# Performance work log

Hardware: AMD Instinct MI355X
Metric: run time of the kernel (lower is better)

The kernel has to match this reference:

```python
import jax, jax.numpy as jnp
import numpy as np
from jax import lax

N, D_IN, D_H, D_A, N_CLS, K = 50000, 1024, 512, 256, 2, 8


def setup_inputs() -> dict:
    key = jax.random.key(0)
    ks = jax.random.split(key, 13)
    s = 0.02
    return {
        "h": jax.random.normal(ks[0], (1, N, D_IN), dtype=jnp.float32),
        "fc_W": jax.random.normal(ks[1], (D_H, D_IN), dtype=jnp.float32) * s,
        "fc_b": jnp.zeros((D_H,), jnp.float32),
        "att_a_W": jax.random.normal(ks[2], (D_A, D_H), dtype=jnp.float32) * s,
        "att_a_b": jnp.zeros((D_A,), jnp.float32),
        "att_b_W": jax.random.normal(ks[3], (D_A, D_H), dtype=jnp.float32) * s,
        "att_b_b": jnp.zeros((D_A,), jnp.float32),
        "att_c_W": jax.random.normal(ks[4], (1, D_A), dtype=jnp.float32) * s,
        "att_c_b": jnp.zeros((1,), jnp.float32),
        "cls_W": jax.random.normal(ks[5], (N_CLS, D_H), dtype=jnp.float32) * s,
        "cls_b": jnp.zeros((N_CLS,), jnp.float32),
        "inst_W": jax.random.normal(ks[6], (2, D_H), dtype=jnp.float32) * s,
        "inst_b": jnp.zeros((2,), jnp.float32),
        "label": 1,  # one_hot -> [0,1]: inst_eval runs only for classifier index 1
    }


def reference(h, fc_W, fc_b, att_a_W, att_a_b, att_b_W, att_b_b,
              att_c_W, att_c_b, cls_W, cls_b, inst_W, inst_b, label):
    x = jnp.squeeze(h, 0)                               # [N, 1024]
    hh = jax.nn.relu(x @ fc_W.T + fc_b)                 # [N, 512]
    # gated attention: tanh gate * sigmoid gate -> scalar score per instance
    a = jnp.tanh(hh @ att_a_W.T + att_a_b)              # [N, 256]
    b = jax.nn.sigmoid(hh @ att_b_W.T + att_b_b)        # [N, 256]
    A_raw = (a * b) @ att_c_W.T + att_c_b               # [N, 1]
    A = jax.nn.softmax(A_raw, axis=0)                   # softmax over instances

    # instance eval (label==1, subtyping=False -> only classifier index 1)
    scores = A_raw[:, 0]                                # [N]
    _, top_p_ids = lax.top_k(scores, K)
    _, top_n_ids = lax.top_k(-scores, K)
    ids = jnp.concatenate([top_p_ids, top_n_ids])       # [2K]
    inst = hh[ids]                                      # gather [2K, 512]
    logits = inst @ inst_W.T + inst_b                   # [2K, 2]
    targets = jnp.concatenate([jnp.ones((K,), jnp.int32),
                               jnp.zeros((K,), jnp.int32)])
    logp = jax.nn.log_softmax(logits, axis=-1)
    instance_loss = -jnp.mean(jnp.take_along_axis(logp, targets[:, None], axis=1))

    instance_scores = hh @ cls_W.T + cls_b              # [N, 2]
    preds = (instance_scores * A).sum(axis=0) / A.sum(axis=0)  # [2]
    preds = preds[None, :]                              # [1, 2]
    return preds, instance_scores, A_raw, instance_loss
```

## Files before the change

### kernel.cpp

```cpp
#include <hip/hip_runtime.h>
#include <hip/hip_bf16.h>
#include <math.h>

typedef __bf16 bf16_t;
typedef __bf16 bf16x4 __attribute__((ext_vector_type(4)));
typedef __bf16 bf16x8 __attribute__((ext_vector_type(8)));
typedef float  f32x4  __attribute__((ext_vector_type(4)));

#define NROWS 50000

typedef const __attribute__((address_space(1))) unsigned int* gp_t;
typedef __attribute__((address_space(3))) unsigned int* lp_t;
__device__ __forceinline__ void cp16(void* l, const void* g) {
    __builtin_amdgcn_global_load_lds((gp_t)g, (lp_t)l, 16, 0, 0);
}

__global__ void k_convert(const float* __restrict__ fcW,
                          const float* __restrict__ aW,
                          const float* __restrict__ bW,
                          const float* __restrict__ clsW,
                          bf16_t* __restrict__ permW1, bf16_t* __restrict__ permB2,
                          bf16_t* __restrict__ clsWb) {
    int t = blockIdx.x * 256 + threadIdx.x;
    if (t < 131072) {
        float4 v = *(const float4*)(fcW + (long)t * 4);
        int row = t >> 8;
        int k0 = (t & 255) * 4;
        int kt = k0 >> 5, q = (k0 >> 3) & 3, j = k0 & 7;
        bf16_t o[4] = {(bf16_t)v.x, (bf16_t)v.y, (bf16_t)v.z, (bf16_t)v.w};
        *(bf16x4*)(permW1 + kt * 16384 + q * 4096 + row * 8 + j) = *(bf16x4*)o;
    } else if (t < 196608) {
        int t2 = t - 131072;
        int isB = t2 >> 15;
        int f = t2 & 32767;
        float4 v = *(const float4*)(((isB ? bW : aW)) + (long)f * 4);
        int srow = f >> 7;
        int k0 = (f & 127) * 4;
        int kt = k0 >> 5, q = (k0 >> 3) & 3, j = k0 & 7;
        int r = ((srow >> 4) * 2 + isB) * 16 + (srow & 15);
        bf16_t o[4] = {(bf16_t)v.x, (bf16_t)v.y, (bf16_t)v.z, (bf16_t)v.w};
        *(bf16x4*)(permB2 + kt * 16384 + q * 4096 + r * 8 + j) = *(bf16x4*)o;
    } else if (t < 197632) {
        int i = t - 196608;
        clsWb[i] = (bf16_t)clsW[i];
    }
}

__global__ __launch_bounds__(256, 4) void k_gemm1(
        const float* __restrict__ x, const bf16_t* __restrict__ permW1,
        const float* __restrict__ fcb, bf16_t* __restrict__ hh) {
    __shared__ __align__(16) char smem[32768];
    const int tid = threadIdx.x;
    const int w = tid >> 6, l = tid & 63, q = l >> 4, li = l & 15;
    const int wr = w >> 1, wc = w & 1;
    const int b = blockIdx.x;
    const int rtile = (b & 7) | ((b >> 5) << 3);
    const int ctile = (b >> 3) & 3;
    const long row0 = (long)rtile * 128;
    const int col0 = ctile * 128;

    f32x4 acc[4][4];
    #pragma unroll
    for (int a = 0; a < 4; a++)
        #pragma unroll
        for (int c = 0; c < 4; c++) acc[a][c] = (f32x4)0.0f;

    int arow[4], akx[4]; bool avalid[4];
    #pragma unroll
    for (int j = 0; j < 4; j++) {
        int s = j * 256 + tid;
        arow[j] = s >> 3; akx[j] = s & 7;
        avalid[j] = (row0 + arow[j]) < NROWS;
    }
    const float* xbase = x + row0 * 1024;

    float4 xv[4];
    #pragma unroll
    for (int j = 0; j < 4; j++)
        xv[j] = avalid[j] ? *(const float4*)(xbase + arow[j] * 1024 + akx[j] * 4)
                          : make_float4(0.f, 0.f, 0.f, 0.f);
    #pragma unroll
    for (int j = 0; j < 4; j++) {
        bf16_t o[4] = {(bf16_t)xv[j].x, (bf16_t)xv[j].y, (bf16_t)xv[j].z, (bf16_t)xv[j].w};
        *(bf16x4*)(smem + (akx[j] >> 1) * 2048 + arow[j] * 16 + (akx[j] & 1) * 8) = *(bf16x4*)o;
    }
    #pragma unroll
    for (int s2 = 0; s2 < 2; s2++) {
        int s = tid + s2 * 256;
        cp16(smem + 16384 + s * 16, permW1 + (s >> 7) * 4096 + (col0 + (s & 127)) * 8);
    }
    #pragma unroll
    for (int j = 0; j < 4; j++)
        xv[j] = avalid[j] ? *(const float4*)(xbase + arow[j] * 1024 + 32 + akx[j] * 4)
                          : make_float4(0.f, 0.f, 0.f, 0.f);
    __syncthreads();

    for (int kt = 0; kt < 32; kt++) {
        const int cur = kt & 1, nxt = cur ^ 1;
        if (kt < 31) {
            const bf16_t* gsrc = permW1 + (long)(kt + 1) * 16384;
            #pragma unroll
            for (int s2 = 0; s2 < 2; s2++) {
                int s = tid + s2 * 256;
                cp16(smem + 16384 + nxt * 8192 + s * 16, gsrc + (s >> 7) * 4096 + (col0 + (s & 127)) * 8);
            }
            #pragma unroll
            for (int j = 0; j < 4; j++) {
                bf16_t o[4] = {(bf16_t)xv[j].x, (bf16_t)xv[j].y, (bf16_t)xv[j].z, (bf16_t)xv[j].w};
                *(bf16x4*)(smem + nxt * 8192 + (akx[j] >> 1) * 2048 + arow[j] * 16 + (akx[j] & 1) * 8) = *(bf16x4*)o;
            }
            int kn = (kt < 30 ? kt + 2 : 31) * 32;
            #pragma unroll
            for (int j = 0; j < 4; j++)
                xv[j] = avalid[j] ? *(const float4*)(xbase + arow[j] * 1024 + kn + akx[j] * 4)
                                  : make_float4(0.f, 0.f, 0.f, 0.f);
        }
        const bf16_t* Ab = (const bf16_t*)(smem + cur * 8192);
        const bf16_t* Bb = (const bf16_t*)(smem + 16384 + cur * 8192);
        bf16x8 afr[4], bfr[4];
        #pragma unroll
        for (int tn = 0; tn < 4; tn++)
            bfr[tn] = *(const bf16x8*)(Bb + q * 1024 + (wc * 64 + tn * 16 + li) * 8);
        #pragma unroll
        for (int tm = 0; tm < 4; tm++)
            afr[tm] = *(const bf16x8*)(Ab + q * 1024 + (wr * 64 + tm * 16 + li) * 8);
        #pragma unroll
        for (int tm = 0; tm < 4; tm++)
            #pragma unroll
            for (int tn = 0; tn < 4; tn++)
                acc[tm][tn] = __builtin_amdgcn_mfma_f32_16x16x32_bf16(afr[tm], bfr[tn], acc[tm][tn], 0, 0, 0);
        __syncthreads();
    }

    bf16_t* t16 = (bf16_t*)smem;
    float bias[4];
    #pragma unroll
    for (int tn = 0; tn < 4; tn++) bias[tn] = fcb[col0 + wc * 64 + tn * 16 + li];
    const int rr = tid >> 3, cc = tid & 7;
    #pragma unroll
    for (int tm = 0; tm < 4; tm++) {
        #pragma unroll
        for (int tn = 0; tn < 4; tn++)
            #pragma unroll
            for (int r = 0; r < 4; r++) {
                float v = acc[tm][tn][r] + bias[tn];
                v = v > 0.f ? v : 0.f;
                t16[(wr * 16 + q * 4 + r) * 136 + wc * 64 + tn * 16 + li] = (bf16_t)v;
            }
        __syncthreads();
        long grow = row0 + ((rr >> 4) * 64) + tm * 16 + (rr & 15);
        if (grow < NROWS) {
            bf16x8 v0 = *(const bf16x8*)&t16[rr * 136 + cc * 16];
            bf16x8 v1 = *(const bf16x8*)&t16[rr * 136 + cc * 16 + 8];
            *(bf16x8*)&hh[grow * 512 + col0 + cc * 16] = v0;
            *(bf16x8*)&hh[grow * 512 + col0 + cc * 16 + 8] = v1;
        }
        __syncthreads();
    }
}

__global__ __launch_bounds__(256, 2) void k_gemm2(
        const bf16_t* __restrict__ hh, const bf16_t* __restrict__ permB2,
        const bf16_t* __restrict__ clsWb,
        const float* __restrict__ aab, const float* __restrict__ abb,
        const float* __restrict__ acW, const float* __restrict__ acb,
        const float* __restrict__ clsb,
        float* __restrict__ Araw, float* __restrict__ inst) {
    __shared__ __align__(16) char smem[51200];
    bf16_t* clsLds = (bf16_t*)(smem + 49152);

    const int tid = threadIdx.x;
    const int w = tid >> 6, l = tid & 63, q = l >> 4, li = l & 15;
    const int wr = w >> 1, wc = w & 1;
    const int b = blockIdx.x;
    const int half = (b >= 391) ? 1 : 0;
    const long row0 = (long)(half ? b - 391 : b) * 128;

    f32x4 acc[4][8];
    #pragma unroll
    for (int a = 0; a < 4; a++)
        #pragma unroll
        for (int c = 0; c < 8; c++) acc[a][c] = (f32x4)0.0f;
    float cls0[4] = {0.f,0.f,0.f,0.f}, cls1[4] = {0.f,0.f,0.f,0.f};

    if (tid < 128) cp16(smem + 49152 + tid * 16, clsWb + tid * 8);
    #pragma unroll
    for (int j = 0; j < 4; j++) {
        int s = j * 256 + tid;
        cp16(smem + 16384 + s * 16, permB2 + (s >> 8) * 4096 + (half * 256 + (s & 255)) * 8);
    }
    #pragma unroll
    for (int j = 0; j < 2; j++) {
        int s = j * 256 + tid;
        cp16(smem + s * 16, hh + (row0 + (s >> 2)) * 512 + (s & 3) * 8);
    }
    __syncthreads();

    for (int kt = 0; kt < 16; kt++) {
        const int cur = kt & 1, nxt = cur ^ 1;
        if (kt < 15) {
            const bf16_t* gb = permB2 + (long)(kt + 1) * 16384;
            #pragma unroll
            for (int j = 0; j < 4; j++) {
                int s = j * 256 + tid;
                cp16(smem + 16384 + nxt * 16384 + s * 16, gb + (s >> 8) * 4096 + (half * 256 + (s & 255)) * 8);
            }
            #pragma unroll
            for (int j = 0; j < 2; j++) {
                int s = j * 256 + tid;
                cp16(smem + nxt * 8192 + s * 16, hh + (row0 + (s >> 2)) * 512 + (kt + 1) * 32 + (s & 3) * 8);
            }
        }
        const bf16_t* Ab = (const bf16_t*)(smem + cur * 8192);
        const bf16_t* Bb = (const bf16_t*)(smem + 16384 + cur * 16384);
        bf16x8 bfr[8];
        #pragma unroll
        for (int tn = 0; tn < 8; tn++)
            bfr[tn] = *(const bf16x8*)(Bb + q * 2048 + (wc * 128 + tn * 16 + li) * 8);
        bf16x8 afr[4];
        #pragma unroll
        for (int tm = 0; tm < 4; tm++)
            afr[tm] = *(const bf16x8*)(Ab + (wr * 64 + tm * 16 + li) * 32 + q * 8);
        #pragma unroll
        for (int tm = 0; tm < 4; tm++)
            #pragma unroll
            for (int tn = 0; tn < 8; tn++)
                acc[tm][tn] = __builtin_amdgcn_mfma_f32_16x16x32_bf16(afr[tm], bfr[tn], acc[tm][tn], 0, 0, 0);
        if (half == 0 && wc == (kt >> 3)) {
            bf16x8 w0 = *(const bf16x8*)(clsLds + kt * 32 + q * 8);
            bf16x8 w1 = *(const bf16x8*)(clsLds + 512 + kt * 32 + q * 8);
            #pragma unroll
            for (int tm = 0; tm < 4; tm++) {
                float s0 = 0.f, s1 = 0.f;
                #pragma unroll
                for (int jj = 0; jj < 8; jj++) {
                    float a = (float)afr[tm][jj];
                    s0 += a * (float)w0[jj];
                    s1 += a * (float)w1[jj];
                }
                cls0[tm] += s0; cls1[tm] += s1;
            }
        }
        __syncthreads();
    }

    float (*apart)[2]     = (float (*)[2])smem;
    float (*cpart)[64][2] = (float (*)[64][2])(smem + 2048);

    float sum_mr[4][4];
    #pragma unroll
    for (int a = 0; a < 4; a++)
        #pragma unroll
        for (int c = 0; c < 4; c++) sum_mr[a][c] = 0.f;
    #pragma unroll
    for (int p = 0; p < 4; p++) {
        int j = (half * 8 + wc * 4 + p) * 16 + li;
        float ab_ = aab[j], bb_ = abb[j], cw = acW[j];
        int tn_a = p * 2, tn_b = p * 2 + 1;
        #pragma unroll
        for (int tm = 0; tm < 4; tm++)
            #pragma unroll
            for (int r = 0; r < 4; r++) {
                float av = tanhf(acc[tm][tn_a][r] + ab_);
                float bv = acc[tm][tn_b][r] + bb_;
                bv = 1.f / (1.f + expf(-bv));
                sum_mr[tm][r] += av * bv * cw;
            }
    }
    #pragma unroll
    for (int tm = 0; tm < 4; tm++)
        #pragma unroll
        for (int r = 0; r < 4; r++) {
            float v = sum_mr[tm][r];
            v += __shfl_xor(v, 1); v += __shfl_xor(v, 2);
            v += __shfl_xor(v, 4); v += __shfl_xor(v, 8);
            if (li == 0) apart[wr * 64 + tm * 16 + q * 4 + r][wc] = v;
        }
    if (half == 0) {
        #pragma unroll
        for (int tm = 0; tm < 4; tm++) {
            cls0[tm] += __shfl_xor(cls0[tm], 16); cls0[tm] += __shfl_xor(cls0[tm], 32);
            cls1[tm] += __shfl_xor(cls1[tm], 16); cls1[tm] += __shfl_xor(cls1[tm], 32);
            if (q == 0) {
                cpart[w][tm * 16 + li][0] = cls0[tm];
                cpart[w][tm * 16 + li][1] = cls1[tm];
            }
        }
    }
    __syncthreads();
    if (tid < 128) {
        float s = apart[tid][0] + apart[tid][1];
        if (half == 0) s += acb[0];
        long row = row0 + tid;
        if (row < NROWS) atomicAdd(Araw + row, s);
    }
    if (half == 0) {
        int r = tid >> 1, c = tid & 1;
        float s = clsb[c] + cpart[2 * (r >> 6)][r & 63][c] + cpart[2 * (r >> 6) + 1][r & 63][c];
        long row = row0 + r;
        if (row < NROWS) inst[row * 2 + c] = s;
    }
}

__global__ void k_topk_part(const float* __restrict__ scores,
                            float* __restrict__ candV, int* __restrict__ candI,
                            float* __restrict__ sums) {
    __shared__ float cv[4096];
    __shared__ int   ci[4096];
    int tid = threadIdx.x;
    int p = blockIdx.x;
    int pass = p & 1, rq = p >> 1;
    if (p == 0 && tid == 0) { sums[0] = 0.f; sums[1] = 0.f; sums[2] = 0.f; }
    float sign = pass ? -1.f : 1.f;
    int lo = rq * 12500, hi = lo + 12500;
    float tv[8]; int ti[8];
    #pragma unroll
    for (int k = 0; k < 8; k++) { tv[k] = -1e30f; ti[k] = 0x7fffffff; }
    for (int i = lo + tid; i < hi; i += 512) {
        float v = sign * scores[i];
        if (v > tv[7] || (v == tv[7] && i < ti[7])) {
            int k = 7;
            while (k > 0 && (v > tv[k-1] || (v == tv[k-1] && i < ti[k-1]))) {
                tv[k] = tv[k-1]; ti[k] = ti[k-1]; k--;
            }
            tv[k] = v; ti[k] = i;
        }
    }
    #pragma unroll
    for (int k = 0; k < 8; k++) { cv[tid * 8 + k] = tv[k]; ci[tid * 8 + k] = ti[k]; }
    __syncthreads();
    if (tid < 64) {
        float mv[8]; int mi[8];
        #pragma unroll
        for (int k = 0; k < 8; k++) { mv[k] = -1e30f; mi[k] = 0x7fffffff; }
        for (int i = 0; i < 64; i++) {
            int slot = tid * 64 + ((i + tid) & 63);
            float v = cv[slot]; int idx = ci[slot];
            #pragma unroll
            for (int k = 0; k < 8; k++) {
                bool bt = (v > mv[k]) || (v == mv[k] && idx < mi[k]);
                float nv = bt ? v : mv[k];  int ni = bt ? idx : mi[k];
                float ov = bt ? mv[k] : v;  int oi = bt ? mi[k] : idx;
                mv[k] = nv; mi[k] = ni; v = ov; idx = oi;
            }
        }
        for (int r = 0; r < 8; r++) {
            float bv = mv[0]; int bi = mi[0]; int bs = tid;
            for (int m = 1; m < 64; m <<= 1) {
                float ov = __shfl_xor(bv, m); int oi = __shfl_xor(bi, m); int os = __shfl_xor(bs, m);
                if (ov > bv || (ov == bv && oi < bi)) { bv = ov; bi = oi; bs = os; }
            }
            if (tid == 0) {
                candV[pass * 32 + rq * 8 + r] = bv;
                candI[pass * 32 + rq * 8 + r] = bi;
            }
            if (tid == bs) {
                #pragma unroll
                for (int k = 0; k < 7; k++) { mv[k] = mv[k+1]; mi[k] = mi[k+1]; }
                mv[7] = -1e30f; mi[7] = 0x7fffffff;
            }
        }
    }
}

__global__ void k_sum(const float* __restrict__ Araw, const float* __restrict__ inst,
                      const float* __restrict__ candV, float* sums) {
    __shared__ float r0[4], r1[4], r2[4];
    int tid = threadIdx.x;
    float mx = -1e30f;
    #pragma unroll
    for (int p = 0; p < 4; p++) mx = fmaxf(mx, candV[p * 8]);
    float se = 0.f, s0 = 0.f, s1 = 0.f;
    for (int i = blockIdx.x * 256 + tid; i < NROWS; i += 32768) {
        float e = expf(Araw[i] - mx);
        se += e; s0 += inst[2 * i] * e; s1 += inst[2 * i + 1] * e;
    }
    for (int s = 1; s < 64; s <<= 1) {
        se += __shfl_xor(se, s); s0 += __shfl_xor(s0, s); s1 += __shfl_xor(s1, s);
    }
    if ((tid & 63) == 0) { r0[tid >> 6] = se; r1[tid >> 6] = s0; r2[tid >> 6] = s1; }
    __syncthreads();
    if (tid == 0) {
        atomicAdd(&sums[0], r0[0] + r0[1] + r0[2] + r0[3]);
        atomicAdd(&sums[1], r1[0] + r1[1] + r1[2] + r1[3]);
        atomicAdd(&sums[2], r2[0] + r2[1] + r2[2] + r2[3]);
    }
}

__global__ void k_fin(const bf16_t* __restrict__ hh,
                      const float* __restrict__ candV, const int* __restrict__ candI,
                      const float* __restrict__ sums, const float* __restrict__ instW,
                      const float* __restrict__ instb, float* __restrict__ dout) {
    __shared__ int mid[16];
    __shared__ float lg[16][2];
    int tid = threadIdx.x;
    int wv = tid >> 6, l = tid & 63;
    if (wv < 2) {
        float v; int idx;
        if (l < 32) { v = candV[wv * 32 + l]; idx = candI[wv * 32 + l]; }
        else        { v = -1e30f; idx = 0x7fffffff; }
        for (int r = 0; r < 8; r++) {
            float bv = v; int bi = idx; int bs = l;
            for (int m = 1; m < 64; m <<= 1) {
                float ov = __shfl_xor(bv, m); int oi = __shfl_xor(bi, m); int os = __shfl_xor(bs, m);
                if (ov > bv || (ov == bv && oi < bi)) { bv = ov; bi = oi; bs = os; }
            }
            if (l == 0) mid[wv * 8 + r] = bi;
            if (l == bs) { v = -1e30f; idx = 0x7fffffff; }
        }
    }
    __syncthreads();
    int r = tid >> 4, li = tid & 15;
    int id = mid[r];
    const bf16_t* hp = hh + (long)id * 512;
    float p0 = 0.f, p1 = 0.f;
    for (int k = li * 32; k < li * 32 + 32; k++) {
        float h = (float)hp[k];
        p0 += h * instW[k]; p1 += h * instW[512 + k];
    }
    for (int m = 1; m < 16; m <<= 1) { p0 += __shfl_xor(p0, m); p1 += __shfl_xor(p1, m); }
    if (li == 0) { lg[r][0] = p0 + instb[0]; lg[r][1] = p1 + instb[1]; }
    __syncthreads();
    if (tid == 0) {
        float loss = 0.f;
        for (int r2 = 0; r2 < 16; r2++) {
            float l0 = lg[r2][0], l1 = lg[r2][1];
            float mx = fmaxf(l0, l1);
            float lse = mx + logf(expf(l0 - mx) + expf(l1 - mx));
            float lt = (r2 < 8) ? l1 : l0;
            loss += (lse - lt);
        }
        dout[150002] = loss / 16.f;
        float se = sums[0];
        dout[0] = sums[1] / se;
        dout[1] = sums[2] / se;
    }
}

extern "C" void kernel_launch(void* const* d_in, const int* in_sizes, int n_in,
                              void* d_out, int out_size, void* d_ws, size_t ws_size,
                              hipStream_t stream) {
    const float* h   = (const float*)d_in[0];
    const float* fcW = (const float*)d_in[1];
    const float* fcb = (const float*)d_in[2];
    const float* aaW = (const float*)d_in[3];
    const float* aab = (const float*)d_in[4];
    const float* abW = (const float*)d_in[5];
    const float* abb = (const float*)d_in[6];
    const float* acW = (const float*)d_in[7];
    const float* acb = (const float*)d_in[8];
    const float* clW = (const float*)d_in[9];
    const float* clb = (const float*)d_in[10];
    const float* inW = (const float*)d_in[11];
    const float* inb = (const float*)d_in[12];
    float* out = (float*)d_out;

    char* ws = (char*)d_ws;
    bf16_t* hh      = (bf16_t*)(ws);
    bf16_t* permW1  = (bf16_t*)(ws + 51200000);
    bf16_t* permB2  = (bf16_t*)(ws + 52248576);
    bf16_t* clsWb   = (bf16_t*)(ws + 52772864);
    float*  candV   = (float*) (ws + 52774912);
    int*    candI   = (int*)   (ws + 52775424);
    float*  sums    = (float*) (ws + 52775936);

    float* inst = out + 2;
    float* Araw = out + 2 + 100000;

    k_convert<<<772, 256, 0, stream>>>(fcW, aaW, abW, clW, permW1, permB2, clsWb);
    k_gemm1<<<1568, 256, 0, stream>>>(h, permW1, fcb, hh);
    hipMemsetAsync(Araw, 0, NROWS * sizeof(float), stream);
    k_gemm2<<<782, 256, 0, stream>>>(hh, permB2, clsWb, aab, abb, acW, acb, clb, Araw, inst);
    k_topk_part<<<8, 512, 0, stream>>>(Araw, candV, candI, sums);
    k_sum<<<128, 256, 0, stream>>>(Araw, inst, candV, sums);
    k_fin<<<1, 256, 0, stream>>>(hh, candV, candI, sums, inW, inb, out);
}
```

Before: 485.3 us.

## Fuse both GEMMs into one kernel keeping hidden tile in LDS

Merges the first GEMM (x→hh) and the attention/classifier GEMM into a single kernel. Each 512-thread block computes a full 128×512 hidden tile, keeps it in LDS, and consumes it directly, so the 51 MB hh round trip through global memory and the Araw memset/atomics go away. Weight B-fragments are now read straight from global/L2 rather than staged in LDS. Instance logits are also computed per row inside the fused kernel, so the final kernel only gathers them. In exchange, the ~146 KB LDS footprint limits occupancy, only 391 blocks are launched, and the uncached global weight loads sit directly in the MFMA loop.

```diff
diff --git a/kernel.cpp b/kernel.cpp
--- a/kernel.cpp
+++ b/kernel.cpp
@@ -9,18 +9,13 @@
 
 #define NROWS 50000
 
-typedef const __attribute__((address_space(1))) unsigned int* gp_t;
-typedef __attribute__((address_space(3))) unsigned int* lp_t;
-__device__ __forceinline__ void cp16(void* l, const void* g) {
-    __builtin_amdgcn_global_load_lds((gp_t)g, (lp_t)l, 16, 0, 0);
-}
-
 __global__ void k_convert(const float* __restrict__ fcW,
                           const float* __restrict__ aW,
                           const float* __restrict__ bW,
                           const float* __restrict__ clsW,
+                          const float* __restrict__ instW,
                           bf16_t* __restrict__ permW1, bf16_t* __restrict__ permB2,
-                          bf16_t* __restrict__ clsWb) {
+                          bf16_t* __restrict__ clsWb, bf16_t* __restrict__ instWb) {
     int t = blockIdx.x * 256 + threadIdx.x;
     if (t < 131072) {
         float4 v = *(const float4*)(fcW + (long)t * 4);
@@ -43,209 +38,152 @@
     } else if (t < 197632) {
         int i = t - 196608;
         clsWb[i] = (bf16_t)clsW[i];
-    }
-}
-
-__global__ __launch_bounds__(256, 4) void k_gemm1(
-        const float* __restrict__ x, const bf16_t* __restrict__ permW1,
-        const float* __restrict__ fcb, bf16_t* __restrict__ hh) {
-    __shared__ __align__(16) char smem[32768];
+    } else if (t < 198656) {
+        int i = t - 197632;
+        instWb[i] = (bf16_t)instW[i];
+    }
+}
+
+__global__ __launch_bounds__(512, 2) void k_fused(
+        const float* __restrict__ x,
+        const bf16_t* __restrict__ permW1, const bf16_t* __restrict__ permB2,
+        const bf16_t* __restrict__ clsWb, const bf16_t* __restrict__ instWb,
+        const float* __restrict__ fcb,
+        const float* __restrict__ aab, const float* __restrict__ abb,
+        const float* __restrict__ acW, const float* __restrict__ acb,
+        const float* __restrict__ clsb, const float* __restrict__ instb,
+        float* __restrict__ Araw, float* __restrict__ inst,
+        float* __restrict__ instLog) {
+    __shared__ __align__(16) char smem[149504];
+    bf16_t* hhT = (bf16_t*)(smem + 16384);
+
     const int tid = threadIdx.x;
     const int w = tid >> 6, l = tid & 63, q = l >> 4, li = l & 15;
-    const int wr = w >> 1, wc = w & 1;
-    const int b = blockIdx.x;
-    const int rtile = (b & 7) | ((b >> 5) << 3);
-    const int ctile = (b >> 3) & 3;
-    const long row0 = (long)rtile * 128;
-    const int col0 = ctile * 128;
-
-    f32x4 acc[4][4];
+    const int wr = w >> 2, wc = w & 3;
+    const long row0 = (long)blockIdx.x * 128;
+
+    f32x4 acc[4][8];
     #pragma unroll
     for (int a = 0; a < 4; a++)
         #pragma unroll
-        for (int c = 0; c < 4; c++) acc[a][c] = (f32x4)0.0f;
-
-    int arow[4], akx[4]; bool avalid[4];
-    #pragma unroll
-    for (int j = 0; j < 4; j++) {
-        int s = j * 256 + tid;
+        for (int c = 0; c < 8; c++) acc[a][c] = (f32x4)0.0f;
+
+    int arow[2], akx[2]; bool av[2];
+    #pragma unroll
+    for (int j = 0; j < 2; j++) {
+        int s = j * 512 + tid;
         arow[j] = s >> 3; akx[j] = s & 7;
-        avalid[j] = (row0 + arow[j]) < NROWS;
-    }
-    const float* xbase = x + row0 * 1024;
-
-    float4 xv[4];
-    #pragma unroll
-    for (int j = 0; j < 4; j++)
-        xv[j] = avalid[j] ? *(const float4*)(xbase + arow[j] * 1024 + akx[j] * 4)
-                          : make_float4(0.f, 0.f, 0.f, 0.f);
-    #pragma unroll
-    for (int j = 0; j < 4; j++) {
+        av[j] = (row0 + arow[j]) < NROWS;
+    }
+    const float* xb = x + row0 * 1024;
+
+    float4 xv[2];
+    #pragma unroll
+    for (int j = 0; j < 2; j++)
+        xv[j] = av[j] ? *(const float4*)(xb + (long)arow[j] * 1024 + akx[j] * 4)
+                      : make_float4(0.f, 0.f, 0.f, 0.f);
+    #pragma unroll
+    for (int j = 0; j < 2; j++) {
         bf16_t o[4] = {(bf16_t)xv[j].x, (bf16_t)xv[j].y, (bf16_t)xv[j].z, (bf16_t)xv[j].w};
         *(bf16x4*)(smem + (akx[j] >> 1) * 2048 + arow[j] * 16 + (akx[j] & 1) * 8) = *(bf16x4*)o;
     }
     #pragma unroll
-    for (int s2 = 0; s2 < 2; s2++) {
-        int s = tid + s2 * 256;
-        cp16(smem + 16384 + s * 16, permW1 + (s >> 7) * 4096 + (col0 + (s & 127)) * 8);
-    }
-    #pragma unroll
-    for (int j = 0; j < 4; j++)
-        xv[j] = avalid[j] ? *(const float4*)(xbase + arow[j] * 1024 + 32 + akx[j] * 4)
-                          : make_float4(0.f, 0.f, 0.f, 0.f);
+    for (int j = 0; j < 2; j++)
+        xv[j] = av[j] ? *(const float4*)(xb + (long)arow[j] * 1024 + 32 + akx[j] * 4)
+                      : make_float4(0.f, 0.f, 0.f, 0.f);
     __syncthreads();
 
     for (int kt = 0; kt < 32; kt++) {
         const int cur = kt & 1, nxt = cur ^ 1;
         if (kt < 31) {
-            const bf16_t* gsrc = permW1 + (long)(kt + 1) * 16384;
-            #pragma unroll
-            for (int s2 = 0; s2 < 2; s2++) {
-                int s = tid + s2 * 256;
-                cp16(smem + 16384 + nxt * 8192 + s * 16, gsrc + (s >> 7) * 4096 + (col0 + (s & 127)) * 8);
-            }
-            #pragma unroll
-            for (int j = 0; j < 4; j++) {
+            #pragma unroll
+            for (int j = 0; j < 2; j++) {
                 bf16_t o[4] = {(bf16_t)xv[j].x, (bf16_t)xv[j].y, (bf16_t)xv[j].z, (bf16_t)xv[j].w};
                 *(bf16x4*)(smem + nxt * 8192 + (akx[j] >> 1) * 2048 + arow[j] * 16 + (akx[j] & 1) * 8) = *(bf16x4*)o;
             }
             int kn = (kt < 30 ? kt + 2 : 31) * 32;
             #pragma unroll
-            for (int j = 0; j < 4; j++)
-                xv[j] = avalid[j] ? *(const float4*)(xbase + arow[j] * 1024 + kn + akx[j] * 4)
-                                  : make_float4(0.f, 0.f, 0.f, 0.f);
+            for (int j = 0; j < 2; j++)
+                xv[j] = av[j] ? *(const float4*)(xb + (long)arow[j] * 1024 + kn + akx[j] * 4)
+                              : make_float4(0.f, 0.f, 0.f, 0.f);
         }
         const bf16_t* Ab = (const bf16_t*)(smem + cur * 8192);
-        const bf16_t* Bb = (const bf16_t*)(smem + 16384 + cur * 8192);
-        bf16x8 afr[4], bfr[4];
-        #pragma unroll
-        for (int tn = 0; tn < 4; tn++)
-            bfr[tn] = *(const bf16x8*)(Bb + q * 1024 + (wc * 64 + tn * 16 + li) * 8);
+        const bf16_t* Bg = permW1 + kt * 16384 + q * 4096;
+        bf16x8 bfr[8], afr[4];
+        #pragma unroll
+        for (int tn = 0; tn < 8; tn++)
+            bfr[tn] = *(const bf16x8*)(Bg + (wc * 128 + tn * 16 + li) * 8);
         #pragma unroll
         for (int tm = 0; tm < 4; tm++)
             afr[tm] = *(const bf16x8*)(Ab + q * 1024 + (wr * 64 + tm * 16 + li) * 8);
         #pragma unroll
         for (int tm = 0; tm < 4; tm++)
             #pragma unroll
-            for (int tn = 0; tn < 4; tn++)
+            for (int tn = 0; tn < 8; tn++)
                 acc[tm][tn] = __builtin_amdgcn_mfma_f32_16x16x32_bf16(afr[tm], bfr[tn], acc[tm][tn], 0, 0, 0);
         __syncthreads();
     }
 
-    bf16_t* t16 = (bf16_t*)smem;
-    float bias[4];
-    #pragma unroll
-    for (int tn = 0; tn < 4; tn++) bias[tn] = fcb[col0 + wc * 64 + tn * 16 + li];
-    const int rr = tid >> 3, cc = tid & 7;
-    #pragma unroll
-    for (int tm = 0; tm < 4; tm++) {
-        #pragma unroll
-        for (int tn = 0; tn < 4; tn++)
-            #pragma unroll
-            for (int r = 0; r < 4; r++) {
-                float v = acc[tm][tn][r] + bias[tn];
-                v = v > 0.f ? v : 0.f;
-                t16[(wr * 16 + q * 4 + r) * 136 + wc * 64 + tn * 16 + li] = (bf16_t)v;
-            }
-        __syncthreads();
-        long grow = row0 + ((rr >> 4) * 64) + tm * 16 + (rr & 15);
-        if (grow < NROWS) {
-            bf16x8 v0 = *(const bf16x8*)&t16[rr * 136 + cc * 16];
-            bf16x8 v1 = *(const bf16x8*)&t16[rr * 136 + cc * 16 + 8];
-            *(bf16x8*)&hh[grow * 512 + col0 + cc * 16] = v0;
-            *(bf16x8*)&hh[grow * 512 + col0 + cc * 16 + 8] = v1;
-        }
-        __syncthreads();
-    }
-}
-
-__global__ __launch_bounds__(256, 2) void k_gemm2(
-        const bf16_t* __restrict__ hh, const bf16_t* __restrict__ permB2,
-        const bf16_t* __restrict__ clsWb,
-        const float* __restrict__ aab, const float* __restrict__ abb,
-        const float* __restrict__ acW, const float* __restrict__ acb,
-        const float* __restrict__ clsb,
-        float* __restrict__ Araw, float* __restrict__ inst) {
-    __shared__ __align__(16) char smem[51200];
-    bf16_t* clsLds = (bf16_t*)(smem + 49152);
-
-    const int tid = threadIdx.x;
-    const int w = tid >> 6, l = tid & 63, q = l >> 4, li = l & 15;
-    const int wr = w >> 1, wc = w & 1;
-    const int b = blockIdx.x;
-    const int half = (b >= 391) ? 1 : 0;
-    const long row0 = (long)(half ? b - 391 : b) * 128;
-
-    f32x4 acc[4][8];
+    {
+        float bias[8];
+        #pragma unroll
+        for (int tn = 0; tn < 8; tn++) bias[tn] = fcb[wc * 128 + tn * 16 + li];
+        #pragma unroll
+        for (int tm = 0; tm < 4; tm++)
+            #pragma unroll
+            for (int tn = 0; tn < 8; tn++)
+                #pragma unroll
+                for (int r = 0; r < 4; r++) {
+                    float v = acc[tm][tn][r] + bias[tn];
+                    v = v > 0.f ? v : 0.f;
+                    hhT[(wr * 64 + tm * 16 + q * 4 + r) * 520 + wc * 128 + tn * 16 + li] = (bf16_t)v;
+                }
+    }
+    __syncthreads();
+
     #pragma unroll
     for (int a = 0; a < 4; a++)
         #pragma unroll
         for (int c = 0; c < 8; c++) acc[a][c] = (f32x4)0.0f;
-    float cls0[4] = {0.f,0.f,0.f,0.f}, cls1[4] = {0.f,0.f,0.f,0.f};
-
-    if (tid < 128) cp16(smem + 49152 + tid * 16, clsWb + tid * 8);
-    #pragma unroll
-    for (int j = 0; j < 4; j++) {
-        int s = j * 256 + tid;
-        cp16(smem + 16384 + s * 16, permB2 + (s >> 8) * 4096 + (half * 256 + (s & 255)) * 8);
-    }
-    #pragma unroll
-    for (int j = 0; j < 2; j++) {
-        int s = j * 256 + tid;
-        cp16(smem + s * 16, hh + (row0 + (s >> 2)) * 512 + (s & 3) * 8);
-    }
-    __syncthreads();
+    float c0[4] = {0,0,0,0}, c1[4] = {0,0,0,0}, c2[4] = {0,0,0,0}, c3[4] = {0,0,0,0};
 
     for (int kt = 0; kt < 16; kt++) {
-        const int cur = kt & 1, nxt = cur ^ 1;
-        if (kt < 15) {
-            const bf16_t* gb = permB2 + (long)(kt + 1) * 16384;
-            #pragma unroll
-            for (int j = 0; j < 4; j++) {
-                int s = j * 256 + tid;
-                cp16(smem + 16384 + nxt * 16384 + s * 16, gb + (s >> 8) * 4096 + (half * 256 + (s & 255)) * 8);
-            }
-            #pragma unroll
-            for (int j = 0; j < 2; j++) {
-                int s = j * 256 + tid;
-                cp16(smem + nxt * 8192 + s * 16, hh + (row0 + (s >> 2)) * 512 + (kt + 1) * 32 + (s & 3) * 8);
-            }
-        }
-        const bf16_t* Ab = (const bf16_t*)(smem + cur * 8192);
-        const bf16_t* Bb = (const bf16_t*)(smem + 16384 + cur * 16384);
-        bf16x8 bfr[8];
+        const bf16_t* Bg = permB2 + kt * 16384 + q * 4096;
+        bf16x8 bfr[8], afr[4];
         #pragma unroll
         for (int tn = 0; tn < 8; tn++)
-            bfr[tn] = *(const bf16x8*)(Bb + q * 2048 + (wc * 128 + tn * 16 + li) * 8);
-        bf16x8 afr[4];
-        #pragma unroll
-        for (int tm = 0; tm < 4; tm++)
-            afr[tm] = *(const bf16x8*)(Ab + (wr * 64 + tm * 16 + li) * 32 + q * 8);
+            bfr[tn] = *(const bf16x8*)(Bg + (wc * 128 + tn * 16 + li) * 8);
+        #pragma unroll
+        for (int tm = 0; tm < 4; tm++)
+            afr[tm] = *(const bf16x8*)(hhT + (wr * 64 + tm * 16 + li) * 520 + kt * 32 + q * 8);
         #pragma unroll
         for (int tm = 0; tm < 4; tm++)
             #pragma unroll
             for (int tn = 0; tn < 8; tn++)
                 acc[tm][tn] = __builtin_amdgcn_mfma_f32_16x16x32_bf16(afr[tm], bfr[tn], acc[tm][tn], 0, 0, 0);
-        if (half == 0 && wc == (kt >> 3)) {
-            bf16x8 w0 = *(const bf16x8*)(clsLds + kt * 32 + q * 8);
-            bf16x8 w1 = *(const bf16x8*)(clsLds + 512 + kt * 32 + q * 8);
+        if ((kt >> 2) == wc) {
+            bf16x8 w0 = *(const bf16x8*)(clsWb + kt * 32 + q * 8);
+            bf16x8 w1 = *(const bf16x8*)(clsWb + 512 + kt * 32 + q * 8);
+            bf16x8 w2 = *(const bf16x8*)(instWb + kt * 32 + q * 8);
+            bf16x8 w3 = *(const bf16x8*)(instWb + 512 + kt * 32 + q * 8);
             #pragma unroll
             for (int tm = 0; tm < 4; tm++) {
-                float s0 = 0.f, s1 = 0.f;
+                float s0 = 0.f, s1 = 0.f, s2 = 0.f, s3 = 0.f;
                 #pragma unroll
                 for (int jj = 0; jj < 8; jj++) {
                     float a = (float)afr[tm][jj];
                     s0 += a * (float)w0[jj];
                     s1 += a * (float)w1[jj];
+                    s2 += a * (float)w2[jj];
+                    s3 += a * (float)w3[jj];
                 }
-                cls0[tm] += s0; cls1[tm] += s1;
-            }
-        }
-        __syncthreads();
-    }
-
-    float (*apart)[2]     = (float (*)[2])smem;
-    float (*cpart)[64][2] = (float (*)[64][2])(smem + 2048);
+                c0[tm] += s0; c1[tm] += s1; c2[tm] += s2; c3[tm] += s3;
+            }
+        }
+    }
+
+    float (*apart)[4]      = (float (*)[4])smem;
+    float (*cpart)[128][4] = (float (*)[128][4])(smem + 2048);
 
     float sum_mr[4][4];
     #pragma unroll
@@ -254,17 +192,16 @@
         for (int c = 0; c < 4; c++) sum_mr[a][c] = 0.f;
     #pragma unroll
     for (int p = 0; p < 4; p++) {
-        int j = (half * 8 + wc * 4 + p) * 16 + li;
+        int j = (wc * 4 + p) * 16 + li;
         float ab_ = aab[j], bb_ = abb[j], cw = acW[j];
-        int tn_a = p * 2, tn_b = p * 2 + 1;
         #pragma unroll
         for (int tm = 0; tm < 4; tm++)
             #pragma unroll
             for (int r = 0; r < 4; r++) {
-                float av = tanhf(acc[tm][tn_a][r] + ab_);
-                float bv = acc[tm][tn_b][r] + bb_;
-                bv = 1.f / (1.f + expf(-bv));
-                sum_mr[tm][r] += av * bv * cw;
+                float avv = tanhf(acc[tm][2 * p][r] + ab_);
+                float bvv = acc[tm][2 * p + 1][r] + bb_;
+                bvv = 1.f / (1.f + expf(-bvv));
+                sum_mr[tm][r] += avv * bvv * cw;
             }
     }
     #pragma unroll
@@ -276,29 +213,34 @@
             v += __shfl_xor(v, 4); v += __shfl_xor(v, 8);
             if (li == 0) apart[wr * 64 + tm * 16 + q * 4 + r][wc] = v;
         }
-    if (half == 0) {
-        #pragma unroll
-        for (int tm = 0; tm < 4; tm++) {
-            cls0[tm] += __shfl_xor(cls0[tm], 16); cls0[tm] += __shfl_xor(cls0[tm], 32);
-            cls1[tm] += __shfl_xor(cls1[tm], 16); cls1[tm] += __shfl_xor(cls1[tm], 32);
-            if (q == 0) {
-                cpart[w][tm * 16 + li][0] = cls0[tm];
-                cpart[w][tm * 16 + li][1] = cls1[tm];
-            }
-        }
-    }
-    __syncthreads();
+    #pragma unroll
+    for (int tm = 0; tm < 4; tm++) {
+        float v0 = c0[tm], v1 = c1[tm], v2 = c2[tm], v3 = c3[tm];
+        v0 += __shfl_xor(v0, 16); v0 += __shfl_xor(v0, 32);
+        v1 += __shfl_xor(v1, 16); v1 += __shfl_xor(v1, 32);
+        v2 += __shfl_xor(v2, 16); v2 += __shfl_xor(v2, 32);
+        v3 += __shfl_xor(v3, 16); v3 += __shfl_xor(v3, 32);
+        if (l < 16) {
+            float* cp = cpart[wc][wr * 64 + tm * 16 + li];
+            cp[0] = v0; cp[1] = v1; cp[2] = v2; cp[3] = v3;
+        }
+    }
+    __syncthreads();
+
     if (tid < 128) {
-        float s = apart[tid][0] + apart[tid][1];
-        if (half == 0) s += acb[0];
-        long row = row0 + tid;
-        if (row < NROWS) atomicAdd(Araw + row, s);
-    }
-    if (half == 0) {
-        int r = tid >> 1, c = tid & 1;
-        float s = clsb[c] + cpart[2 * (r >> 6)][r & 63][c] + cpart[2 * (r >> 6) + 1][r & 63][c];
-        long row = row0 + r;
-        if (row < NROWS) inst[row * 2 + c] = s;
+        long g = row0 + tid;
+        if (g < NROWS) {
+            float s = apart[tid][0] + apart[tid][1] + apart[tid][2] + apart[tid][3] + acb[0];
+            Araw[g] = s;
+            float o0 = clsb[0], o1 = clsb[1], o2 = instb[0], o3 = instb[1];
+            #pragma unroll
+            for (int k = 0; k < 4; k++) {
+                o0 += cpart[k][tid][0]; o1 += cpart[k][tid][1];
+                o2 += cpart[k][tid][2]; o3 += cpart[k][tid][3];
+            }
+            inst[g * 2]     = o0; inst[g * 2 + 1]     = o1;
+            instLog[g * 2]  = o2; instLog[g * 2 + 1]  = o3;
+        }
     }
 }
 
@@ -387,12 +329,10 @@
     }
 }
 
-__global__ void k_fin(const bf16_t* __restrict__ hh,
+__global__ void k_fin(const float* __restrict__ instLog,
                       const float* __restrict__ candV, const int* __restrict__ candI,
-                      const float* __restrict__ sums, const float* __restrict__ instW,
-                      const float* __restrict__ instb, float* __restrict__ dout) {
+                      const float* __restrict__ sums, float* __restrict__ dout) {
     __shared__ int mid[16];
-    __shared__ float lg[16][2];
     int tid = threadIdx.x;
     int wv = tid >> 6, l = tid & 63;
     if (wv < 2) {
@@ -410,30 +350,20 @@
         }
     }
     __syncthreads();
-    int r = tid >> 4, li = tid & 15;
-    int id = mid[r];
-    const bf16_t* hp = hh + (long)id * 512;
-    float p0 = 0.f, p1 = 0.f;
-    for (int k = li * 32; k < li * 32 + 32; k++) {
-        float h = (float)hp[k];
-        p0 += h * instW[k]; p1 += h * instW[512 + k];
-    }
-    for (int m = 1; m < 16; m <<= 1) { p0 += __shfl_xor(p0, m); p1 += __shfl_xor(p1, m); }
-    if (li == 0) { lg[r][0] = p0 + instb[0]; lg[r][1] = p1 + instb[1]; }
-    __syncthreads();
-    if (tid == 0) {
-        float loss = 0.f;
-        for (int r2 = 0; r2 < 16; r2++) {
-            float l0 = lg[r2][0], l1 = lg[r2][1];
-            float mx = fmaxf(l0, l1);
-            float lse = mx + logf(expf(l0 - mx) + expf(l1 - mx));
-            float lt = (r2 < 8) ? l1 : l0;
-            loss += (lse - lt);
-        }
-        dout[150002] = loss / 16.f;
-        float se = sums[0];
-        dout[0] = sums[1] / se;
-        dout[1] = sums[2] / se;
+    if (tid < 16) {
+        int id = mid[tid];
+        float l0 = instLog[id * 2], l1 = instLog[id * 2 + 1];
+        float mx = fmaxf(l0, l1);
+        float lse = mx + logf(expf(l0 - mx) + expf(l1 - mx));
+        float lt = (tid < 8) ? l1 : l0;
+        float term = lse - lt;
+        for (int m = 1; m < 16; m <<= 1) term += __shfl_xor(term, m);
+        if (tid == 0) {
+            dout[150002] = term / 16.f;
+            float se = sums[0];
+            dout[0] = sums[1] / se;
+            dout[1] = sums[2] / se;
+        }
     }
 }
 
@@ -456,22 +386,23 @@
     float* out = (float*)d_out;
 
     char* ws = (char*)d_ws;
-    bf16_t* hh      = (bf16_t*)(ws);
-    bf16_t* permW1  = (bf16_t*)(ws + 51200000);
-    bf16_t* permB2  = (bf16_t*)(ws + 52248576);
-    bf16_t* clsWb   = (bf16_t*)(ws + 52772864);
-    float*  candV   = (float*) (ws + 52774912);
-    int*    candI   = (int*)   (ws + 52775424);
-    float*  sums    = (float*) (ws + 52775936);
+    bf16_t* permW1  = (bf16_t*)(ws);
+    bf16_t* permB2  = (bf16_t*)(ws + 1048576);
+    bf16_t* clsWb   = (bf16_t*)(ws + 1572864);
+    bf16_t* instWb  = (bf16_t*)(ws + 1574912);
+    float*  instLog = (float*) (ws + 1576960);
+    float*  candV   = (float*) (ws + 1976960);
+    int*    candI   = (int*)   (ws + 1977216);
+    float*  sums    = (float*) (ws + 1977472);
 
     float* inst = out + 2;
     float* Araw = out + 2 + 100000;
 
-    k_convert<<<772, 256, 0, stream>>>(fcW, aaW, abW, clW, permW1, permB2, clsWb);
-    k_gemm1<<<1568, 256, 0, stream>>>(h, permW1, fcb, hh);
-    hipMemsetAsync(Araw, 0, NROWS * sizeof(float), stream);
-    k_gemm2<<<782, 256, 0, stream>>>(hh, permB2, clsWb, aab, abb, acW, acb, clb, Araw, inst);
+    k_convert<<<776, 256, 0, stream>>>(fcW, aaW, abW, clW, inW, permW1, permB2, clsWb, instWb);
+    k_fused<<<391, 512, 0, stream>>>(h, permW1, permB2, clsWb, instWb,
+                                     fcb, aab, abb, acW, acb, clb, inb,
+                                     Araw, inst, instLog);
     k_topk_part<<<8, 512, 0, stream>>>(Araw, candV, candI, sums);
     k_sum<<<128, 256, 0, stream>>>(Araw, inst, candV, sums);
-    k_fin<<<1, 256, 0, stream>>>(hh, candV, candI, sums, inW, inb, out);
-}
+    k_fin<<<1, 128, 0, stream>>>(instLog, candV, candI, sums, out);
+}
```

New measurement: 492.4 us. About the same (+1.4%).
